# Kernel optimization log

Measured on AMD Instinct MI355X. Metric: run time of the kernel, lower is better.

Reference implementation:

```python
import jax, jax.numpy as jnp
import numpy as np

T, B, D, BF = 512, 256, 256, 2  # time (nodes/tree), batch, feature dim, branching factor


def setup_inputs() -> dict:
    key = jax.random.key(0)
    k1, k2, k3 = jax.random.split(key, 3)
    inputs = jax.random.normal(k1, (T, B, D), dtype=jnp.float32)
    # Valid postfix (shift-reduce) arity sequence: two leaves, then alternate
    # combine(2)/leaf(0) -> left-comb binary tree; keeps stack pointer in range.
    t = np.arange(T)
    ar = np.where((t >= 2) & (t % 2 == 0), 2, 0).astype(np.int64)
    arities = jnp.asarray(np.broadcast_to(ar[:, None], (T, B)))
    scale = 1.0 / np.sqrt(D)
    W_in = jax.random.normal(k2, (D, D), dtype=jnp.float32) * scale
    W_ch = jax.random.normal(k3, (BF, D, D), dtype=jnp.float32) * scale
    b = jnp.zeros((D,), dtype=jnp.float32)
    return {"inputs": inputs, "arities": arities, "W_in": W_in, "W_ch": W_ch, "b": b}


def reference(inputs, arities, W_in, W_ch, b):
    Tn, Bn, Dn = inputs.shape
    bf = W_ch.shape[0]
    k = jnp.arange(Bn)

    def unit(x, children):
        # tree-RNN cell: tanh(x@W_in + sum_i child_i@W_ch[i] + b)
        h = x @ W_in + b
        for i in range(bf):
            h = h + children[i] @ W_ch[i]
        return jnp.tanh(h)

    memory0 = jnp.zeros((Tn, Bn, Dn), dtype=inputs.dtype)
    stack0 = jnp.zeros((Bn, Tn + bf), dtype=arities.dtype)
    ptr0 = jnp.full((Bn,), bf - 1, dtype=arities.dtype)

    def step(carry, xs):
        memory, stack, ptr = carry
        x_t, ar, t = xs
        children = []
        for i in range(bf):
            idx = stack[k, ptr - i]                    # [B] top-of-stack pointers
            entry = memory[idx, k]                     # [B, D] gather child features
            mask = (ar > i).astype(entry.dtype)[:, None]
            children.append(entry * mask)              # zero absent children
        new_entry = unit(x_t, children)
        memory = memory.at[t].set(new_entry)           # scatter to memory slot t
        ptr = ptr - jnp.abs(ar) + 1                    # pop arity, push 1
        ignore = ar == -1
        # stack[k,ptr] *= ignore; += t*(1-ignore)  <=>  keep old if ignore else t
        stack = stack.at[k, ptr].set(jnp.where(ignore, stack[k, ptr], t))
        return (memory, stack, ptr), None

    (memory, stack, ptr), _ = jax.lax.scan(
        step, (memory0, stack0, ptr0), (inputs, arities, jnp.arange(Tn)))
    out = memory[stack[k, ptr], k]                     # [B, D] tree roots
    return (out, memory)
```

## Files before the change

kernel.cpp:

```cpp
#include <hip/hip_runtime.h>
#include <hip/hip_bf16.h>


constexpr int T = 512, B = 256, D = 256;

constexpr int WS_CNT  = 0;
constexpr int WS_ROOT = 16;
constexpr int WS_NW   = 272;
constexpr int WS_L0   = 1024;
constexpr int WS_L1   = WS_L0 + T * B;
constexpr int WS_WORK = WS_L1 + T * B;

__global__ __launch_bounds__(256) void k_stack(const int* __restrict__ ar,
                                               unsigned* __restrict__ ws) {
  __shared__ int ar_l[T];
  __shared__ int S[1024];
  __shared__ unsigned lbuf0[T];
  __shared__ unsigned lbuf1[T];
  __shared__ unsigned wbuf[1024];
  __shared__ int cnts[4];
  __shared__ unsigned base0, base1;

  int k = blockIdx.x;
  int tid = threadIdx.x;
  ar_l[tid]       = ar[tid * B + k];
  ar_l[tid + 256] = ar[(tid + 256) * B + k];
  S[tid] = 0; S[tid + 256] = 0; S[tid + 512] = 0; S[tid + 768] = 0;
  __syncthreads();

  if (tid == 0) {
    int ptr = 1;
    int top = 0, next = 0;
    int n0 = 0, n1 = 0, nw = 0;
    for (int t = 0; t < T; t++) {
      int a = ar_l[t];
      int aa = a < 0 ? -a : a;
      unsigned cc[2]; int ncc = 0;
      if (a > 0) {
        int c0 = top;
        if (ar_l[c0] <= 0)
          lbuf0[n0++] = (unsigned)c0 | ((unsigned)t << 9) | ((unsigned)k << 18);
        else
          cc[ncc++] = (unsigned)c0;
        if (a > 1) {
          int c1 = next;
          if (ar_l[c1] <= 0)
            lbuf1[n1++] = (unsigned)c1 | ((unsigned)t << 9) | ((unsigned)k << 18);
          else
            cc[ncc++] = (unsigned)c1 | (1u << 18);
        }
      }
      if (a >= 1) {
        if (ncc == 0) {
          wbuf[nw++] = (unsigned)t | (1u << 19) | (1u << 20);
        } else {
          for (int e = 0; e < ncc; e++) {
            unsigned w = (unsigned)t | ((cc[e] & 511u) << 9) |
                         (((cc[e] >> 18) & 1u) << 18) | (1u << 21);
            if (e == 0) w |= (1u << 19);
            if (e == ncc - 1) w |= (1u << 20);
            wbuf[nw++] = w;
          }
        }
      }
      int pnew = ptr - aa + 1;
      if (a != -1) {
        S[pnew & 1023] = t;
        if (aa == 0)      { next = top; top = t; }
        else if (aa == 1) { top = t; }
        else              { top = t; next = S[(pnew - 1) & 1023]; }
      }
      ptr = pnew;
    }
    cnts[0] = n0; cnts[1] = n1; cnts[2] = nw;
    cnts[3] = S[ptr & 1023];
    base0 = atomicAdd(ws + WS_CNT + 0, (unsigned)n0);
    base1 = atomicAdd(ws + WS_CNT + 1, (unsigned)n1);
  }
  __syncthreads();
  int n0 = cnts[0], n1 = cnts[1], nw = cnts[2];
  for (int i = tid; i < n0; i += 256) ws[WS_L0 + base0 + i] = lbuf0[i];
  for (int i = tid; i < n1; i += 256) ws[WS_L1 + base1 + i] = lbuf1[i];
  for (int i = tid; i < nw; i += 256) ws[WS_WORK + k * 1024 + i] = wbuf[i];
  if (tid == 0) { ws[WS_NW + k] = (unsigned)nw; ws[WS_ROOT + k] = (unsigned)cnts[3]; }
}

__global__ __launch_bounds__(256) void k_gemm_h(const float* __restrict__ X,
                                                const float* __restrict__ W,
                                                const float* __restrict__ bias,
                                                float* __restrict__ Hm) {
  int row0 = blockIdx.x * 64;
  __shared__ float As[16][65];
  __shared__ float Bs[16][256];
  int tid = threadIdx.x;
  int cq = tid & 31, rg = tid >> 5;
  float acc[8][8];
#pragma unroll
  for (int q = 0; q < 8; q++) {
    float bv = bias[cq + 32 * q];
#pragma unroll
    for (int rr = 0; rr < 8; rr++) acc[rr][q] = bv;
  }
  int sr = tid >> 2;
  int skc = (tid & 3) * 4;
  for (int kk = 0; kk < 256; kk += 16) {
    float4 a4 = *(const float4*)&X[(row0 + sr) * 256 + kk + skc];
    As[skc + 0][sr] = a4.x; As[skc + 1][sr] = a4.y;
    As[skc + 2][sr] = a4.z; As[skc + 3][sr] = a4.w;
#pragma unroll
    for (int r = 0; r < 16; r++) Bs[r][tid] = W[(kk + r) * 256 + tid];
    __syncthreads();
#pragma unroll
    for (int kc = 0; kc < 16; kc++) {
      float a[8], bb[8];
#pragma unroll
      for (int rr = 0; rr < 8; rr++) a[rr] = As[kc][rg * 8 + rr];
#pragma unroll
      for (int q = 0; q < 8; q++) bb[q] = Bs[kc][cq + 32 * q];
#pragma unroll
      for (int rr = 0; rr < 8; rr++)
#pragma unroll
        for (int q = 0; q < 8; q++) acc[rr][q] += a[rr] * bb[q];
    }
    __syncthreads();
  }
#pragma unroll
  for (int rr = 0; rr < 8; rr++)
#pragma unroll
    for (int q = 0; q < 8; q++)
      Hm[(row0 + rg * 8 + rr) * 256 + cq + 32 * q] = acc[rr][q];
}

__global__ __launch_bounds__(256) void k_leafgemm(const float* __restrict__ Hm,
                                                  float* __restrict__ Gm,
                                                  const float* __restrict__ Wch,
                                                  const unsigned* __restrict__ list,
                                                  const unsigned* __restrict__ cntp,
                                                  int which) {
  unsigned cnt = *cntp;
  unsigned tile0 = blockIdx.x * 64;
  if (tile0 >= cnt) return;
  int ne = (int)min(64u, cnt - tile0);
  __shared__ unsigned ent[64];
  __shared__ float As[16][65];
  __shared__ float Bs[16][256];
  int tid = threadIdx.x;
  if (tid < 64) ent[tid] = (tid < ne) ? list[tile0 + tid] : 0u;
  __syncthreads();
  const float* W = Wch + which * (D * D);
  int cq = tid & 31, rg = tid >> 5;
  float acc[8][8];
#pragma unroll
  for (int rr = 0; rr < 8; rr++)
#pragma unroll
    for (int q = 0; q < 8; q++) acc[rr][q] = 0.0f;
  int sr = tid >> 2;
  int skc = (tid & 3) * 4;
  unsigned se = ent[sr];
  int sc = (int)(se & 511u), skb = (int)((se >> 18) & 255u);
  const float* srow = &Hm[((sc << 8) + skb) * 256];
  for (int kk = 0; kk < 256; kk += 16) {
    float4 a4;
    if (sr < ne) a4 = *(const float4*)&srow[kk + skc];
    else { a4.x = a4.y = a4.z = a4.w = 0.0f; }
    As[skc + 0][sr] = tanhf(a4.x); As[skc + 1][sr] = tanhf(a4.y);
    As[skc + 2][sr] = tanhf(a4.z); As[skc + 3][sr] = tanhf(a4.w);
#pragma unroll
    for (int r = 0; r < 16; r++) Bs[r][tid] = W[(kk + r) * 256 + tid];
    __syncthreads();
#pragma unroll
    for (int kc = 0; kc < 16; kc++) {
      float a[8], bb[8];
#pragma unroll
      for (int rr = 0; rr < 8; rr++) a[rr] = As[kc][rg * 8 + rr];
#pragma unroll
      for (int q = 0; q < 8; q++) bb[q] = Bs[kc][cq + 32 * q];
#pragma unroll
      for (int rr = 0; rr < 8; rr++)
#pragma unroll
        for (int q = 0; q < 8; q++) acc[rr][q] += a[rr] * bb[q];
    }
    __syncthreads();
  }
#pragma unroll
  for (int rr = 0; rr < 8; rr++) {
    int e = rg * 8 + rr;
    if (e < ne) {
      unsigned en = ent[e];
      int t = (int)((en >> 9) & 511u), kb = (int)((en >> 18) & 255u);
      float* dst = &Gm[((t << 8) + kb) * 256];
#pragma unroll
      for (int q = 0; q < 8; q++) dst[cq + 32 * q] += acc[rr][q];
    }
  }
}

__global__ __launch_bounds__(256) void k_leaftanh(const int* __restrict__ ar,
                                                  float* __restrict__ Mm) {
  int r0 = blockIdx.x * 64;
  __shared__ int lar[64];
  int tid = threadIdx.x;
  if (tid < 64) lar[tid] = ar[r0 + tid];
  __syncthreads();
  for (int r = 0; r < 64; r++) {
    if (lar[r] <= 0) {
      float v = Mm[(r0 + r) * 256 + tid];
      Mm[(r0 + r) * 256 + tid] = tanhf(v);
    }
  }
}

__global__ __launch_bounds__(512) void k_seq(float* __restrict__ Mm,
                                             const float* __restrict__ Wch,
                                             const unsigned* __restrict__ ws) {
  int k = blockIdx.x;
  int tid = threadIdx.x;
  int j = tid & 255, h = tid >> 8;
  __shared__ __align__(16) float crow[256];
  __shared__ float partial[256];
  __shared__ int cached;
  if (tid == 0) cached = -1;
  float w[128];
  const float* W1 = Wch + D * D;
#pragma unroll
  for (int p = 0; p < 128; p++) w[p] = W1[(h * 128 + p) * 256 + j];
  int nw = (int)ws[WS_NW + k];
  const unsigned* work = ws + WS_WORK + k * 1024;
  float acc = 0.0f;
  __syncthreads();
  for (int n = 0; n < nw; n++) {
    unsigned e = work[n];
    int t = (int)(e & 511u), c = (int)((e >> 9) & 511u);
    int wi = (int)((e >> 18) & 1u);
    bool first = (e >> 19) & 1u, last = (e >> 20) & 1u, hasc = (e >> 21) & 1u;
    if (first) acc = (h == 0) ? Mm[((t << 8) + k) * 256 + j] : 0.0f;
    if (hasc) {
      if (c != cached) {
        __syncthreads();
        if (tid < 256) crow[tid] = Mm[((c << 8) + k) * 256 + tid];
        if (tid == 0) cached = c;
        __syncthreads();
      }
      if (wi == 1) {
#pragma unroll
        for (int p = 0; p < 32; p++) {
          float4 c4 = ((const float4*)crow)[h * 32 + p];
          acc += c4.x * w[4 * p] + c4.y * w[4 * p + 1] +
                 c4.z * w[4 * p + 2] + c4.w * w[4 * p + 3];
        }
      } else {
        const float* W0 = Wch;
#pragma unroll 8
        for (int p = 0; p < 128; p++)
          acc += crow[h * 128 + p] * W0[(h * 128 + p) * 256 + j];
      }
    }
    if (last) {
      if (h == 1) partial[j] = acc;
      __syncthreads();
      if (h == 0) {
        float v = tanhf(acc + partial[j]);
        Mm[((t << 8) + k) * 256 + j] = v;
        crow[j] = v;
      }
      if (tid == 0) cached = t;
      __syncthreads();
    }
  }
}

__global__ __launch_bounds__(256) void k_root(const float* __restrict__ Mm,
                                              float* __restrict__ out,
                                              const unsigned* __restrict__ ws) {
  int k = blockIdx.x;
  unsigned r = ws[WS_ROOT + k];
  out[k * 256 + threadIdx.x] = Mm[(((int)r << 8) + k) * 256 + threadIdx.x];
}

extern "C" void kernel_launch(void* const* d_in, const int* in_sizes, int n_in,
                              void* d_out, int out_size, void* d_ws, size_t ws_size,
                              hipStream_t stream) {
  const float* X    = (const float*)d_in[0];
  const int*   AR   = (const int*)d_in[1];
  const float* Win  = (const float*)d_in[2];
  const float* Wch  = (const float*)d_in[3];
  const float* bias = (const float*)d_in[4];
  float* out = (float*)d_out;
  float* Mm  = out + B * D;
  unsigned* ws = (unsigned*)d_ws;

  hipMemsetAsync(d_ws, 0, 512, stream);
  k_stack<<<B, 256, 0, stream>>>(AR, ws);
  k_gemm_h<<<(T * B) / 64, 256, 0, stream>>>(X, Win, bias, Mm);
  k_leafgemm<<<(T * B) / 64, 256, 0, stream>>>(Mm, Mm, Wch, ws + WS_L0, ws + WS_CNT + 0, 0);
  k_leafgemm<<<(T * B) / 64, 256, 0, stream>>>(Mm, Mm, Wch, ws + WS_L1, ws + WS_CNT + 1, 1);
  k_leaftanh<<<(T * B) / 64, 256, 0, stream>>>(AR, Mm);
  k_seq<<<B, 512, 0, stream>>>(Mm, Wch, ws);
  k_root<<<B, 256, 0, stream>>>(Mm, out, ws);
}
```

Before: 1.081 ms.

## Use fp16 dot2 weights, readlane broadcast, prefetch, and batched ring writes in sequential kernel

```diff
diff --git a/kernel.cpp b/kernel.cpp
--- a/kernel.cpp
+++ b/kernel.cpp
@@ -3,6 +3,16 @@
 
 
 constexpr int T = 512, B = 256, D = 256;
+
+typedef _Float16 h2 __attribute__((ext_vector_type(2)));
+
+__device__ __forceinline__ float dot2f(h2 a, h2 b, float c) {
+#if __has_builtin(__builtin_amdgcn_fdot2)
+  return __builtin_amdgcn_fdot2(a, b, c, false);
+#else
+  return c + (float)a.x * (float)b.x + (float)a.y * (float)b.y;
+#endif
+}
 
 constexpr int WS_CNT  = 0;
 constexpr int WS_ROOT = 16;
@@ -215,57 +225,103 @@
                                              const unsigned* __restrict__ ws) {
   int k = blockIdx.x;
   int tid = threadIdx.x;
-  int j = tid & 255, h = tid >> 8;
-  __shared__ __align__(16) float crow[256];
+  int j = tid & 255, h = tid >> 8, lane = tid & 63;
+
+  __shared__ unsigned wl[1024];
+  __shared__ _Float16 crow16[256];
   __shared__ float partial[256];
-  __shared__ int cached;
-  if (tid == 0) cached = -1;
-  float w[128];
+  __shared__ float ring[8][256];
+  __shared__ int tstore[8];
+
   const float* W1 = Wch + D * D;
-#pragma unroll
-  for (int p = 0; p < 128; p++) w[p] = W1[(h * 128 + p) * 256 + j];
+  int pbase = h << 7;
+  h2 w[64];
+#pragma unroll 8
+  for (int q = 0; q < 64; q++) {
+    float f0 = W1[(pbase + 2 * q) * 256 + j];
+    float f1 = W1[(pbase + 2 * q + 1) * 256 + j];
+    w[q].x = (_Float16)f0; w[q].y = (_Float16)f1;
+  }
   int nw = (int)ws[WS_NW + k];
-  const unsigned* work = ws + WS_WORK + k * 1024;
-  float acc = 0.0f;
-  __syncthreads();
+  for (int i = tid; i < nw; i += 512) wl[i] = ws[WS_WORK + k * 1024 + i];
+  __syncthreads();
+
+  int cached = -1;
+  int m = 0, flushbase = 0;
+  float gcur = 0.0f;
+  if (nw > 0 && h == 0) {
+    int t0 = (int)(wl[0] & 511u);
+    gcur = Mm[((t0 << 8) + k) * 256 + j];
+  }
+  float a0 = 0.f, a1 = 0.f, a2 = 0.f, a3 = 0.f;
+
   for (int n = 0; n < nw; n++) {
-    unsigned e = work[n];
+    unsigned e = wl[n];
     int t = (int)(e & 511u), c = (int)((e >> 9) & 511u);
     int wi = (int)((e >> 18) & 1u);
     bool first = (e >> 19) & 1u, last = (e >> 20) & 1u, hasc = (e >> 21) & 1u;
-    if (first) acc = (h == 0) ? Mm[((t << 8) + k) * 256 + j] : 0.0f;
+    if (first) { a1 = a2 = a3 = 0.f; a0 = (h == 0) ? gcur : 0.f; }
+    float gnext = 0.0f;
+    if (h == 0 && n + 1 < nw) {
+      int tn = (int)(wl[n + 1] & 511u);
+      gnext = Mm[((tn << 8) + k) * 256 + j];
+    }
     if (hasc) {
       if (c != cached) {
+        int cnt = m - flushbase;
+        for (int i = tid; i < cnt * 256; i += 512) {
+          int r = flushbase + (i >> 8), col = i & 255;
+          Mm[((tstore[r & 7] << 8) + k) * 256 + col] = ring[r & 7][col];
+        }
+        flushbase = m;
         __syncthreads();
-        if (tid < 256) crow[tid] = Mm[((c << 8) + k) * 256 + tid];
-        if (tid == 0) cached = c;
+        if (tid < 256) crow16[tid] = (_Float16)Mm[((c << 8) + k) * 256 + tid];
         __syncthreads();
+        cached = c;
       }
       if (wi == 1) {
-#pragma unroll
-        for (int p = 0; p < 32; p++) {
-          float4 c4 = ((const float4*)crow)[h * 32 + p];
-          acc += c4.x * w[4 * p] + c4.y * w[4 * p + 1] +
-                 c4.z * w[4 * p + 2] + c4.w * w[4 * p + 3];
+        int cpair = ((const int*)crow16)[(h << 6) | lane];
+#pragma unroll
+        for (int p = 0; p < 64; p++) {
+          int cs = __builtin_amdgcn_readlane(cpair, p);
+          union { int i; h2 v; } u; u.i = cs;
+          if ((p & 3) == 0)      a0 = dot2f(w[p], u.v, a0);
+          else if ((p & 3) == 1) a1 = dot2f(w[p], u.v, a1);
+          else if ((p & 3) == 2) a2 = dot2f(w[p], u.v, a2);
+          else                   a3 = dot2f(w[p], u.v, a3);
         }
       } else {
-        const float* W0 = Wch;
-#pragma unroll 8
-        for (int p = 0; p < 128; p++)
-          acc += crow[h * 128 + p] * W0[(h * 128 + p) * 256 + j];
+        for (int p = pbase; p < pbase + 128; p++)
+          a0 += (float)crow16[p] * Wch[p * 256 + j];
       }
     }
     if (last) {
-      if (h == 1) partial[j] = acc;
+      if (h == 1) partial[j] = (a0 + a1) + (a2 + a3);
       __syncthreads();
       if (h == 0) {
-        float v = tanhf(acc + partial[j]);
-        Mm[((t << 8) + k) * 256 + j] = v;
-        crow[j] = v;
-      }
-      if (tid == 0) cached = t;
+        float s = (a0 + a1) + (a2 + a3) + partial[j];
+        float v = tanhf(s);
+        crow16[j] = (_Float16)v;
+        ring[m & 7][j] = v;
+      }
+      if (tid == 0) tstore[m & 7] = t;
+      cached = t;
+      m++;
       __syncthreads();
-    }
+      if ((m & 7) == 0) {
+        for (int i = tid; i < 8 * 256; i += 512) {
+          int r = (m - 8) + (i >> 8), col = i & 255;
+          Mm[((tstore[r & 7] << 8) + k) * 256 + col] = ring[r & 7][col];
+        }
+        flushbase = m;
+      }
+    }
+    gcur = gnext;
+  }
+  int cnt = m - flushbase;
+  for (int i = tid; i < cnt * 256; i += 512) {
+    int r = flushbase + (i >> 8), col = i & 255;
+    Mm[((tstore[r & 7] << 8) + k) * 256 + col] = ring[r & 7][col];
   }
 }
 
```

Result: slower. 1.847 ms (+70.9%).
